# Kernel optimization log

Measured on AMD Instinct MI355X. Metric: run time of the kernel, lower is better.

## Reference

```python
import jax, jax.numpy as jnp
import numpy as np

OUT = 64      # output resolution of torchvision Resize([64, 64])
Y_OFF = 82    # hard-coded vertical offset in the original forward


def _crop_resize(img_i, box):
    # img_i: [H, W, C] float32 ; box: [4] int32 = (x1, y1, x2, y2)
    x1 = box[0]
    y1 = box[1] + Y_OFF
    x2 = box[2]
    y2 = box[3] + Y_OFF
    h = (y2 - y1).astype(jnp.float32)
    w = (x2 - x1).astype(jnp.float32)

    # source coords inside the crop, matching bilinear align_corners=False
    sy = jnp.clip((jnp.arange(OUT, dtype=jnp.float32) + 0.5) * h / OUT - 0.5, 0.0, h - 1.0)
    sx = jnp.clip((jnp.arange(OUT, dtype=jnp.float32) + 0.5) * w / OUT - 0.5, 0.0, w - 1.0)

    y0f = jnp.floor(sy)
    x0f = jnp.floor(sx)
    wy = sy - y0f                     # [64]
    wx = sx - x0f                     # [64]
    y0 = y0f.astype(jnp.int32)
    x0 = x0f.astype(jnp.int32)
    yp = jnp.minimum(y0 + 1, y2 - y1 - 1)
    xp = jnp.minimum(x0 + 1, x2 - x1 - 1)

    gy0, gy1 = y0 + y1, yp + y1       # global row indices
    gx0, gx1 = x0 + x1, xp + x1       # global col indices

    rgb = img_i[..., :3]              # only first 3 channels are cropped

    def gat(gy, gx):
        return rgb[gy[:, None], gx[None, :], :]   # [64, 64, 3]

    wx_ = wx[None, :, None]
    wy_ = wy[:, None, None]
    top = gat(gy0, gx0) * (1.0 - wx_) + gat(gy0, gx1) * wx_
    bot = gat(gy1, gx0) * (1.0 - wx_) + gat(gy1, gx1) * wx_
    out = top * (1.0 - wy_) + bot * wy_            # [64, 64, 3]
    return jnp.transpose(out, (2, 0, 1))           # [3, 64, 64] (CHW like torch)


def setup_inputs() -> dict:
    key = jax.random.key(0)
    k1, k2, k3, k4, k5 = jax.random.split(key, 5)
    B, H, W, C = 64, 644, 640, 3
    img = jax.random.normal(k1, (B, H, W, C), dtype=jnp.float32)
    x1 = jax.random.randint(k2, (B,), 0, 300)
    y1 = jax.random.randint(k3, (B,), 0, 260)
    bw = jax.random.randint(k4, (B,), 64, 300)
    bh = jax.random.randint(k5, (B,), 64, 300)
    bbox = jnp.stack([x1, y1, x1 + bw, y1 + bh], axis=1).astype(jnp.int32)
    return {"img": img, "bbox": bbox}


def reference(img, bbox):
    # batched dynamic crop + bilinear resize to 64x64 (ROIAlign-style)
    return jax.vmap(_crop_resize)(img, bbox)   # [B, 3, 64, 64]
```

## Files before the change

### kernel.cpp

```cpp
#include <hip/hip_runtime.h>
#include <hip/hip_bf16.h>

#define OUT 64
#define YOFF 82
#define IMG_H 644
#define IMG_W 640

__global__ __launch_bounds__(256) void crop_resize_kernel(
    const float* __restrict__ img, const int* __restrict__ bbox,
    float* __restrict__ out)
{
    int idx = blockIdx.x * blockDim.x + threadIdx.x;
    int x = idx & 63;
    int y = (idx >> 6) & 63;
    int b = idx >> 12;

    const int4 bb = ((const int4*)bbox)[b];
    int x1 = bb.x;
    int y1 = bb.y + YOFF;
    int x2 = bb.z;
    int y2 = bb.w + YOFF;
    int hi = y2 - y1;
    int wi = x2 - x1;
    float h = (float)hi;
    float w = (float)wi;

    float sy = ((float)y + 0.5f) * h / 64.0f - 0.5f;
    sy = fminf(fmaxf(sy, 0.0f), h - 1.0f);
    float sx = ((float)x + 0.5f) * w / 64.0f - 0.5f;
    sx = fminf(fmaxf(sx, 0.0f), w - 1.0f);

    float y0f = floorf(sy);
    float x0f = floorf(sx);
    float wy = sy - y0f;
    float wx = sx - x0f;
    int y0 = (int)y0f;
    int x0 = (int)x0f;
    int yp = min(y0 + 1, hi - 1);
    int xp = min(x0 + 1, wi - 1);

    int gy0 = y0 + y1, gy1 = yp + y1;
    int gx0 = x0 + x1, gx1 = xp + x1;

    const float* base = img + (size_t)b * (IMG_H * IMG_W * 3);
    const float* p00 = base + ((size_t)gy0 * IMG_W + gx0) * 3;
    const float* p01 = base + ((size_t)gy0 * IMG_W + gx1) * 3;
    const float* p10 = base + ((size_t)gy1 * IMG_W + gx0) * 3;
    const float* p11 = base + ((size_t)gy1 * IMG_W + gx1) * 3;

    float omwx = 1.0f - wx;
    float omwy = 1.0f - wy;

    float* o = out + (size_t)b * 3 * (OUT * OUT) + y * OUT + x;
#pragma unroll
    for (int c = 0; c < 3; ++c) {
        float top = p00[c] * omwx + p01[c] * wx;
        float bot = p10[c] * omwx + p11[c] * wx;
        o[c * (OUT * OUT)] = top * omwy + bot * wy;
    }
}

extern "C" void kernel_launch(void* const* d_in, const int* in_sizes, int n_in,
                              void* d_out, int out_size, void* d_ws, size_t ws_size,
                              hipStream_t stream) {
    const float* img = (const float*)d_in[0];
    const int* bbox = (const int*)d_in[1];
    float* out = (float*)d_out;

    int total = 64 * OUT * OUT;
    dim3 block(256);
    dim3 grid(total / 256);
    crop_resize_kernel<<<grid, block, 0, stream>>>(img, bbox, out);
}
```

Measured before the change: 10.02 us.

## Stage needed source rows into LDS with coalesced float4 loads before bilinear sampling

Each block now handles 4 output rows of one image. It loads the 8 required source rows (top and bottom for each output row) across the crop width into shared memory with aligned float4 loads, then does the bilinear interpolation from LDS. This replaces scattered per-thread gathers of 12 floats with coalesced row loads. In exchange it reads whole crop rows even where only 64 samples are needed, and adds a barrier and 29 KB of LDS per block, which may reduce occupancy.

Measured after the change: 9.972 us. About the same (-0.5%).

```diff
diff --git a/kernel.cpp b/kernel.cpp
--- a/kernel.cpp
+++ b/kernel.cpp
@@ -5,57 +5,76 @@
 #define YOFF 82
 #define IMG_H 644
 #define IMG_W 640
+#define ROWS 4
+#define RS 904
 
 __global__ __launch_bounds__(256) void crop_resize_kernel(
     const float* __restrict__ img, const int* __restrict__ bbox,
     float* __restrict__ out)
 {
-    int idx = blockIdx.x * blockDim.x + threadIdx.x;
-    int x = idx & 63;
-    int y = (idx >> 6) & 63;
-    int b = idx >> 12;
+    __shared__ float lds[2 * ROWS * RS];
+    int tid = threadIdx.x;
+    int b = blockIdx.x >> 4;
+    int yo_base = (blockIdx.x & 15) * ROWS;
 
     const int4 bb = ((const int4*)bbox)[b];
-    int x1 = bb.x;
-    int y1 = bb.y + YOFF;
-    int x2 = bb.z;
-    int y2 = bb.w + YOFF;
-    int hi = y2 - y1;
-    int wi = x2 - x1;
-    float h = (float)hi;
-    float w = (float)wi;
+    int x1 = bb.x, y1 = bb.y + YOFF, x2 = bb.z, y2 = bb.w + YOFF;
+    int hi = y2 - y1, wi = x2 - x1;
+    float h = (float)hi, w = (float)wi;
 
-    float sy = ((float)y + 0.5f) * h / 64.0f - 0.5f;
+    const float* base = img + (size_t)b * (IMG_H * IMG_W * 3);
+
+#pragma unroll
+    for (int r8 = 0; r8 < 2 * ROWS; ++r8) {
+        int r = r8 >> 1;
+        int yo = yo_base + r;
+        float sy = ((float)yo + 0.5f) * h / 64.0f - 0.5f;
+        sy = fminf(fmaxf(sy, 0.0f), h - 1.0f);
+        int y0 = (int)floorf(sy);
+        int gy = ((r8 & 1) ? min(y0 + 1, hi - 1) : y0) + y1;
+        int rowstart = (gy * IMG_W + x1) * 3;
+        int astart = rowstart & ~3;
+        int shift = rowstart & 3;
+        int n_dw = wi * 3 + shift;
+        int i = tid * 4;
+        if (i < n_dw) {
+            float4 v = *(const float4*)(base + astart + i);
+            *(float4*)&lds[r8 * RS + i] = v;
+        }
+    }
+    __syncthreads();
+
+    int r = tid >> 6;
+    int x = tid & 63;
+    int yo = yo_base + r;
+
+    float sy = ((float)yo + 0.5f) * h / 64.0f - 0.5f;
     sy = fminf(fmaxf(sy, 0.0f), h - 1.0f);
+    float y0f = floorf(sy);
+    float wy = sy - y0f;
+    int y0i = (int)y0f;
+
     float sx = ((float)x + 0.5f) * w / 64.0f - 0.5f;
     sx = fminf(fmaxf(sx, 0.0f), w - 1.0f);
-
-    float y0f = floorf(sy);
     float x0f = floorf(sx);
-    float wy = sy - y0f;
     float wx = sx - x0f;
-    int y0 = (int)y0f;
     int x0 = (int)x0f;
-    int yp = min(y0 + 1, hi - 1);
     int xp = min(x0 + 1, wi - 1);
 
-    int gy0 = y0 + y1, gy1 = yp + y1;
-    int gx0 = x0 + x1, gx1 = xp + x1;
+    int gy0 = y0i + y1;
+    int gy1 = min(y0i + 1, hi - 1) + y1;
+    int sh0 = ((gy0 * IMG_W + x1) * 3) & 3;
+    int sh1 = ((gy1 * IMG_W + x1) * 3) & 3;
 
-    const float* base = img + (size_t)b * (IMG_H * IMG_W * 3);
-    const float* p00 = base + ((size_t)gy0 * IMG_W + gx0) * 3;
-    const float* p01 = base + ((size_t)gy0 * IMG_W + gx1) * 3;
-    const float* p10 = base + ((size_t)gy1 * IMG_W + gx0) * 3;
-    const float* p11 = base + ((size_t)gy1 * IMG_W + gx1) * 3;
+    const float* r0 = &lds[(2 * r) * RS + sh0];
+    const float* r1 = &lds[(2 * r + 1) * RS + sh1];
 
-    float omwx = 1.0f - wx;
-    float omwy = 1.0f - wy;
-
-    float* o = out + (size_t)b * 3 * (OUT * OUT) + y * OUT + x;
+    float omwx = 1.0f - wx, omwy = 1.0f - wy;
+    float* o = out + (size_t)b * 3 * (OUT * OUT) + yo * OUT + x;
 #pragma unroll
     for (int c = 0; c < 3; ++c) {
-        float top = p00[c] * omwx + p01[c] * wx;
-        float bot = p10[c] * omwx + p11[c] * wx;
+        float top = r0[x0 * 3 + c] * omwx + r0[xp * 3 + c] * wx;
+        float bot = r1[x0 * 3 + c] * omwx + r1[xp * 3 + c] * wx;
         o[c * (OUT * OUT)] = top * omwy + bot * wy;
     }
 }
@@ -67,8 +86,7 @@
     const int* bbox = (const int*)d_in[1];
     float* out = (float*)d_out;
 
-    int total = 64 * OUT * OUT;
     dim3 block(256);
-    dim3 grid(total / 256);
+    dim3 grid(64 * (OUT / ROWS));
     crop_resize_kernel<<<grid, block, 0, stream>>>(img, bbox, out);
 }
```
